# Performance work log

Hardware: AMD Instinct MI355X
Metric: run time of the kernel (lower is better)

The kernel has to match this reference:

```python
import jax, jax.numpy as jnp
from jax import lax
import numpy as np

D_MODEL = 2048
NUM_EXPERTS = 16
NUM_TOKENS = 8192  # must be divisible by NUM_EXPERTS (balanced assignment)


def setup_inputs() -> dict:
    key = jax.random.key(0)
    k1, k2 = jax.random.split(key)
    features = jax.random.normal(k1, (NUM_TOKENS, D_MODEL), dtype=jnp.float32)
    # gate weight (orthogonal init in torch; gaussian is fine for a numerical baseline)
    W = jax.random.normal(k2, (NUM_EXPERTS, D_MODEL), dtype=jnp.float32) * 0.1
    b = jnp.zeros((NUM_EXPERTS,), dtype=jnp.float32)
    return {"features": features, "W": W, "b": b, "is_training": 1}


def _balanced_assignment(scores):
    """Greedy balanced assignment: each expert receives exactly T//E tokens.
    Deterministic stand-in for the cpp auction-based balanced_assignment: scan
    over tokens, each token takes its best-scoring expert with remaining capacity.
    Returns sort_by_expert: token indices sorted (stably) by assigned expert."""
    T, E = scores.shape
    cap_per_expert = T // E

    def step(cap, s):  # cap: [E] remaining capacity, s: [E] token's scores
        masked = jnp.where(cap > 0, s, -jnp.inf)
        e = jnp.argmax(masked)
        return cap.at[e].add(-1), e

    _, tok2exp = lax.scan(step, jnp.full((E,), cap_per_expert, dtype=jnp.int32), scores)
    sort_by_expert = jnp.argsort(tok2exp, stable=True)  # [T] token ids grouped by expert
    return sort_by_expert


def reference(features, W, b, is_training):
    # gating computed under no_grad in the original
    affinities = lax.stop_gradient(features @ W.T + b)  # [T, E]
    T, E = affinities.shape
    cap = T // E

    sort_by_expert = _balanced_assignment(affinities)

    routing_probs = jax.nn.softmax(affinities, axis=1)  # [T, E]

    # gather_scores: permute probs into expert order, pick each token's score for
    # its assigned expert, then un-permute back to original token order.
    sorted_probs = routing_probs[sort_by_expert]                 # [T, E]
    expert_idx = (jnp.arange(T) // cap)[:, None]                 # [T, 1], balanced splits
    gathered = jnp.take_along_axis(sorted_probs, expert_idx, axis=1)  # [T, 1]
    i_sort = jnp.argsort(sort_by_expert)                         # inverse permutation
    gathered_scores = gathered[i_sort]                           # [T, 1]

    return sort_by_expert, gathered_scores
```

## Files before the change

### kernel.cpp

```cpp
#include <hip/hip_runtime.h>
#include <hip/hip_bf16.h>
#include <math.h>

#define T_TOK 8192
#define D_MODEL 2048
#define N_EXP 16
#define CAP 512
#define NSEG (T_TOK / 64)
#define KSPLIT 2
#define KRANGE (D_MODEL / KSPLIT)


__device__ __forceinline__ unsigned int f2ord(float f) {
    unsigned int b = __float_as_uint(f);
    return (b & 0x80000000u) ? ~b : (b | 0x80000000u);
}

__global__ __launch_bounds__(256, 2) void gemm_partial_kernel(
    const float* __restrict__ feat, const float* __restrict__ W,
    float* __restrict__ partial)
{
    __shared__ float w_lds[N_EXP * KRANGE];

    const int tid  = threadIdx.x;
    const int wave = tid >> 6, lane = tid & 63;
    const int t0   = (blockIdx.x & 255) * 32;
    const int ks   = blockIdx.x >> 8;
    const int k0   = ks * KRANGE;

    for (int i = tid; i < N_EXP * KRANGE / 4; i += 256) {
        int e = i / (KRANGE / 4), r = i % (KRANGE / 4);
        ((float4*)w_lds)[i] = *(const float4*)(W + (size_t)e * D_MODEL + k0 + r * 4);
    }
    __syncthreads();

    const float* fbase = feat + (size_t)(t0 + wave * 8) * D_MODEL + k0 + lane * 4;

    float acc[128];
    #pragma unroll
    for (int i = 0; i < 128; ++i) acc[i] = 0.f;

    float4 cur[8], nxt[8];
    #pragma unroll
    for (int r = 0; r < 8; ++r)
        cur[r] = *(const float4*)(fbase + (size_t)r * D_MODEL);

    #pragma unroll
    for (int j = 0; j < KRANGE / 256; ++j) {
        if (j < KRANGE / 256 - 1) {
            #pragma unroll
            for (int r = 0; r < 8; ++r)
                nxt[r] = *(const float4*)(fbase + (size_t)r * D_MODEL + (j + 1) * 256);
        }
        const int kbase = j * 256 + lane * 4;
        #pragma unroll
        for (int e = 0; e < N_EXP; ++e) {
            float4 wv = *(const float4*)&w_lds[e * KRANGE + kbase];
            #pragma unroll
            for (int r = 0; r < 8; ++r) {
                acc[r * 16 + e] += cur[r].x * wv.x;
                acc[r * 16 + e] += cur[r].y * wv.y;
                acc[r * 16 + e] += cur[r].z * wv.z;
                acc[r * 16 + e] += cur[r].w * wv.w;
            }
        }
        #pragma unroll
        for (int r = 0; r < 8; ++r) cur[r] = nxt[r];
    }

    #pragma unroll
    for (int step = 0; step < 6; ++step) {
        const int m    = 1 << step;
        const int half = 128 >> (step + 1);
        const bool hi  = (lane & m) != 0;
        #pragma unroll
        for (int jj = 0; jj < half; ++jj) {
            float send = hi ? acc[jj] : acc[jj + half];
            float recv = __shfl_xor(send, m, 64);
            acc[jj] = (hi ? acc[jj + half] : acc[jj]) + recv;
        }
    }
    const int rl = ((lane & 1) << 5) | (((lane >> 1) & 1) << 4) | (((lane >> 2) & 1) << 3)
                 | (((lane >> 3) & 1) << 2) | (((lane >> 4) & 1) << 1) | ((lane >> 5) & 1);
    #pragma unroll
    for (int jj = 0; jj < 2; ++jj) {
        int slot = (rl << 1) | jj;
        int r = slot >> 4, e = slot & 15;
        partial[((size_t)ks * T_TOK + t0 + wave * 8 + r) * N_EXP + e] = acc[jj];
    }
}

__global__ __launch_bounds__(256) void finalize_kernel(
    const float* __restrict__ partial, const float* __restrict__ bias,
    unsigned long long* __restrict__ pref, float* __restrict__ probs,
    unsigned char* __restrict__ choice0, int* __restrict__ cnt0)
{
    const int tid = threadIdx.x;
    const int t = blockIdx.x * 256 + tid;
    const int wave = tid >> 6, lane = tid & 63;

    float aff[N_EXP];
    {
        const float4* p0 = (const float4*)(partial + (size_t)t * N_EXP);
        const float4* p1 = (const float4*)(partial + ((size_t)T_TOK + t) * N_EXP);
        #pragma unroll
        for (int q = 0; q < 4; ++q) {
            float4 a = p0[q], b = p1[q];
            aff[q*4+0] = a.x + b.x; aff[q*4+1] = a.y + b.y;
            aff[q*4+2] = a.z + b.z; aff[q*4+3] = a.w + b.w;
        }
    }
    #pragma unroll
    for (int e = 0; e < N_EXP; ++e) aff[e] += bias[e];

    float m = aff[0];
    #pragma unroll
    for (int e = 1; e < N_EXP; ++e) m = fmaxf(m, aff[e]);
    float s = 0.f;
    #pragma unroll
    for (int e = 0; e < N_EXP; ++e) s += __expf(aff[e] - m);

    float4* pr = (float4*)(probs + (size_t)t * N_EXP);
    #pragma unroll
    for (int q = 0; q < 4; ++q) {
        float4 v;
        v.x = __expf(aff[q*4+0] - m) / s;
        v.y = __expf(aff[q*4+1] - m) / s;
        v.z = __expf(aff[q*4+2] - m) / s;
        v.w = __expf(aff[q*4+3] - m) / s;
        pr[q] = v;
    }

    unsigned long long key[N_EXP];
    #pragma unroll
    for (int j = 0; j < N_EXP; ++j)
        key[j] = ((unsigned long long)f2ord(aff[j]) << 4) | (unsigned long long)(15 - j);
    unsigned long long pk = 0ull;
    unsigned int used = 0;
    for (int r = 0; r < N_EXP; ++r) {
        unsigned long long bk = 0ull; int be = 0;
        for (int j = 0; j < N_EXP; ++j)
            if (!((used >> j) & 1u) && key[j] > bk) { bk = key[j]; be = j; }
        used |= (1u << be);
        pk = (pk << 4) | (unsigned long long)be;
    }
    pref[t] = pk;

    const int c = (int)(pk >> 60);
    choice0[t] = (unsigned char)c;
    #pragma unroll
    for (int e = 0; e < N_EXP; ++e) {
        unsigned long long mm = __ballot(c == e);
        if (lane == e) cnt0[(blockIdx.x * 4 + wave) * N_EXP + e] = (int)__popcll(mm);
    }
}

__global__ __launch_bounds__(512) void events_kernel(
    const unsigned long long* __restrict__ pref,
    const unsigned char* __restrict__ choice0,
    const int* __restrict__ cnt0, int* __restrict__ evt)
{
    __shared__ unsigned char choiceL[T_TOK];
    __shared__ int cnt [NSEG][N_EXP + 1];
    __shared__ int pseg[NSEG][N_EXP + 1];
    __shared__ int rem_cap[N_EXP], fparr[N_EXP], addF[N_EXP];
    __shared__ int s_avail, s_start, s_pmin, s_fe, s_seglo;
    __shared__ int evp[N_EXP], evf[N_EXP];

    const int tid  = threadIdx.x;
    const int wave = tid >> 6, lane = tid & 63;
    const unsigned long long lt_mask = (1ull << lane) - 1ull;

    for (int i = tid; i < T_TOK / 4; i += 512)
        ((unsigned int*)choiceL)[i] = ((const unsigned int*)choice0)[i];
    for (int i = tid; i < NSEG * N_EXP; i += 512)
        cnt[i >> 4][i & 15] = cnt0[i];
    if (tid < N_EXP) rem_cap[tid] = CAP;
    if (tid == 0) { s_avail = 0xFFFF; s_start = 0; s_seglo = 0; }
    __syncthreads();

    for (int round = 0; round < N_EXP; ++round) {
        const int start = s_start;
        const unsigned int avail = (unsigned int)s_avail;
        const int seglo = s_seglo;

        #pragma unroll
        for (int ee = 0; ee < 2; ++ee) {
            const int e = wave + ee * 8;
            const int s0 = 2 * lane, s1 = s0 + 1;
            const int c0 = (s0 >= seglo) ? cnt[s0][e] : 0;
            const int c1 = (s1 >= seglo) ? cnt[s1][e] : 0;
            const int pairsum = c0 + c1;
            int v = pairsum;
            #pragma unroll
            for (int d = 1; d < 64; d <<= 1) {
                int o = __shfl_up(v, d, 64);
                if (lane >= d) v += o;
            }
            const int excl0 = v - pairsum;
            const int excl1 = excl0 + c0;
            pseg[s0][e] = excl0;
            pseg[s1][e] = excl1;

            int fp = 0x7FFFFFFF;
            if ((avail >> e) & 1u) {
                const int need = rem_cap[e];
                int segc = 0x7FFFFFFF, kk = 0;
                if (excl0 < need && excl0 + c0 >= need)      { segc = s0; kk = need - excl0; }
                else if (excl1 < need && excl1 + c1 >= need) { segc = s1; kk = need - excl1; }
                unsigned long long b = __ballot(segc != 0x7FFFFFFF);
                if (b) {
                    int l2    = __builtin_ctzll(b);
                    int sstar = __shfl(segc, l2, 64);
                    int k2    = __shfl(kk,   l2, 64);
                    int t = sstar * 64 + lane;
                    int cc = (t >= start) ? (int)choiceL[t] : -1;
                    unsigned long long m = __ballot(cc == e);
                    int r = (int)__popcll(m & lt_mask);
                    bool hit = ((m >> lane) & 1ull) && (r == k2 - 1);
                    unsigned long long hb = __ballot(hit);
                    fp = sstar * 64 + __builtin_ctzll(hb);
                }
            }
            if (lane == 0) fparr[e] = fp;
        }
        __syncthreads();

        if (tid == 0) {
            int pm = 0x7FFFFFFF, f = 0;
            #pragma unroll
            for (int e = 0; e < N_EXP; ++e)
                if (fparr[e] < pm) { pm = fparr[e]; f = e; }
            s_pmin = pm; s_fe = f;
        }
        __syncthreads();
        const int pmin = s_pmin, fe = s_fe;
        const int segF = pmin >> 6;

        if (wave == 0) {
            int t = segF * 64 + lane;
            int cc = (t >= start && t <= pmin) ? (int)choiceL[t] : -1;
            #pragma unroll
            for (int e = 0; e < N_EXP; ++e) {
                unsigned long long mm = __ballot(cc == e);
                if (lane == e) addF[e] = (int)__popcll(mm);
            }
        }
        __syncthreads();

        if (tid < N_EXP) rem_cap[tid] -= pseg[segF][tid] + addF[tid];
        if (tid == 0) {
            evp[round] = pmin; evf[round] = fe;
            s_avail = (int)(avail & ~(1u << fe));
            s_start = pmin + 1;
            s_seglo = segF;
        }
        __syncthreads();

        if (round < N_EXP - 1) {
            const unsigned int navail = (unsigned int)s_avail;
            for (int t = pmin + 1 + tid; t < T_TOK; t += 512) {
                if ((int)choiceL[t] == fe) {
                    unsigned long long pp = pref[t];
                    int e2 = (int)(pp >> 60);
                    while (!((navail >> e2) & 1u)) { pp <<= 4; e2 = (int)(pp >> 60); }
                    choiceL[t] = (unsigned char)e2;
                }
            }
            __syncthreads();
            for (int s = segF + wave; s < NSEG; s += 8) {
                int t = s * 64 + lane;
                int cc = (t > pmin) ? (int)choiceL[t] : -1;
                #pragma unroll
                for (int e = 0; e < N_EXP; ++e) {
                    unsigned long long mm = __ballot(cc == e);
                    if (lane == e) cnt[s][e] = (int)__popcll(mm);
                }
            }
            __syncthreads();
        }
    }

    if (tid < N_EXP) { evt[tid] = evp[tid]; evt[N_EXP + tid] = evf[tid]; }
}

__global__ __launch_bounds__(256) void choice_kernel(
    const unsigned long long* __restrict__ pref, const int* __restrict__ evt,
    unsigned char* __restrict__ t2e, int* __restrict__ bcnt)
{
    __shared__ int evp[N_EXP], evf[N_EXP];
    __shared__ int sc[4][N_EXP];
    const int tid = threadIdx.x, b = blockIdx.x;
    const int wave = tid >> 6, lane = tid & 63;
    if (tid < N_EXP) evp[tid] = evt[tid];
    else if (tid < 2 * N_EXP) evf[tid - N_EXP] = evt[tid];
    __syncthreads();

    const int t = b * 256 + tid;
    unsigned int mask = 0xFFFFu;
    #pragma unroll
    for (int j = 0; j < N_EXP; ++j)
        if (evp[j] < t) mask &= ~(1u << evf[j]);

    unsigned long long pp = pref[t];
    int e = (int)(pp >> 60);
    while (!((mask >> e) & 1u)) { pp <<= 4; e = (int)(pp >> 60); }
    t2e[t] = (unsigned char)e;

    #pragma unroll
    for (int e2 = 0; e2 < N_EXP; ++e2) {
        unsigned long long mm = __ballot(e == e2);
        if (lane == e2) sc[wave][e2] = (int)__popcll(mm);
    }
    __syncthreads();
    if (tid < N_EXP)
        bcnt[b * N_EXP + tid] = sc[0][tid] + sc[1][tid] + sc[2][tid] + sc[3][tid];
}

__global__ __launch_bounds__(256) void writeout_kernel(
    const unsigned char* __restrict__ t2e, const int* __restrict__ bcnt,
    const float* __restrict__ probs,
    float* __restrict__ out0, float* __restrict__ out1)
{
    __shared__ int base[N_EXP];
    __shared__ int sc[4][N_EXP];
    const int tid = threadIdx.x, b = blockIdx.x;
    const int wave = tid >> 6, lane = tid & 63;
    const unsigned long long lt_mask = (1ull << lane) - 1ull;

    const int t = b * 256 + tid;
    const int c = (int)t2e[t];

    unsigned long long own = 0ull;
    #pragma unroll
    for (int e2 = 0; e2 < N_EXP; ++e2) {
        unsigned long long mm = __ballot(c == e2);
        if (c == e2) own = mm;
        if (lane == e2) sc[wave][e2] = (int)__popcll(mm);
    }
    if (tid < N_EXP) {
        int s = 0;
        for (int b2 = 0; b2 < b; ++b2) s += bcnt[b2 * N_EXP + tid];
        base[tid] = s;
    }
    __syncthreads();

    int rank = (int)__popcll(own & lt_mask);
    for (int w2 = 0; w2 < wave; ++w2) rank += sc[w2][c];
    const int pos = base[c] + rank;
    out0[c * CAP + pos] = (float)t;
    out1[t] = probs[(size_t)t * N_EXP + c];
}

extern "C" void kernel_launch(void* const* d_in, const int* in_sizes, int n_in,
                              void* d_out, int out_size, void* d_ws, size_t ws_size,
                              hipStream_t stream) {
    const float* feat = (const float*)d_in[0];
    const float* W    = (const float*)d_in[1];
    const float* bias = (const float*)d_in[2];

    float* out = (float*)d_out;
    char*  ws  = (char*)d_ws;

    float* partial           = (float*)ws;
    unsigned long long* pref = (unsigned long long*)(ws + 1048576);
    float* probs             = (float*)(ws + 1114112);
    unsigned char* choice0   = (unsigned char*)(ws + 1638400);
    int* cnt0                = (int*)(ws + 1646592);
    int* evt                 = (int*)(ws + 1654784);
    unsigned char* t2e       = (unsigned char*)(ws + 1654912);
    int* bcnt                = (int*)(ws + 1663104);

    hipLaunchKernelGGL(gemm_partial_kernel, dim3(512), dim3(256), 0, stream,
                       feat, W, partial);
    hipLaunchKernelGGL(finalize_kernel, dim3(T_TOK / 256), dim3(256), 0, stream,
                       partial, bias, pref, probs, choice0, cnt0);
    hipLaunchKernelGGL(events_kernel, dim3(1), dim3(512), 0, stream,
                       pref, choice0, cnt0, evt);
    hipLaunchKernelGGL(choice_kernel, dim3(T_TOK / 256), dim3(256), 0, stream,
                       pref, evt, t2e, bcnt);
    hipLaunchKernelGGL(writeout_kernel, dim3(T_TOK / 256), dim3(256), 0, stream,
                       t2e, bcnt, probs, out, out + T_TOK);
}
```

Baseline: 197.8 us.

## Track per-segment expert bitmasks in events kernel and drop GEMM K-split

The single-block events kernel now keeps per-expert 64-bit token bitmasks per segment in LDS, updated with atomicOr when tokens are reassigned. This replaces the byte choice array and the full recount of every segment with ballots each round, cutting the serial per-round work in the one-block critical path. The GEMM no longer splits K in two or stages W in LDS. Each wave does four tokens over the full K range and reads W straight from global/cache, with higher occupancy and no partial-sum buffer, so finalize reads one affinity array. The risk is LDS atomic contention and heavier W traffic through cache.

Result: faster. 191.6 us (-3.1%).

```diff
diff --git a/kernel.cpp b/kernel.cpp
--- a/kernel.cpp
+++ b/kernel.cpp
@@ -7,8 +7,6 @@
 #define N_EXP 16
 #define CAP 512
 #define NSEG (T_TOK / 64)
-#define KSPLIT 2
-#define KRANGE (D_MODEL / KSPLIT)
 
 
 __device__ __forceinline__ unsigned int f2ord(float f) {
@@ -16,62 +14,57 @@
     return (b & 0x80000000u) ? ~b : (b | 0x80000000u);
 }
 
-__global__ __launch_bounds__(256, 2) void gemm_partial_kernel(
+__global__ __launch_bounds__(256, 4) void gemm_aff_kernel(
     const float* __restrict__ feat, const float* __restrict__ W,
-    float* __restrict__ partial)
-{
-    __shared__ float w_lds[N_EXP * KRANGE];
-
+    float* __restrict__ aff)
+{
     const int tid  = threadIdx.x;
     const int wave = tid >> 6, lane = tid & 63;
-    const int t0   = (blockIdx.x & 255) * 32;
-    const int ks   = blockIdx.x >> 8;
-    const int k0   = ks * KRANGE;
-
-    for (int i = tid; i < N_EXP * KRANGE / 4; i += 256) {
-        int e = i / (KRANGE / 4), r = i % (KRANGE / 4);
-        ((float4*)w_lds)[i] = *(const float4*)(W + (size_t)e * D_MODEL + k0 + r * 4);
-    }
-    __syncthreads();
-
-    const float* fbase = feat + (size_t)(t0 + wave * 8) * D_MODEL + k0 + lane * 4;
-
-    float acc[128];
-    #pragma unroll
-    for (int i = 0; i < 128; ++i) acc[i] = 0.f;
-
-    float4 cur[8], nxt[8];
-    #pragma unroll
-    for (int r = 0; r < 8; ++r)
+    const int tbase = blockIdx.x * 16 + wave * 4;
+
+    const float* fbase = feat + (size_t)tbase * D_MODEL + lane * 4;
+
+    float acc[64];
+    #pragma unroll
+    for (int i = 0; i < 64; ++i) acc[i] = 0.f;
+
+    float4 cur[4], nxt[4];
+    #pragma unroll
+    for (int r = 0; r < 4; ++r)
         cur[r] = *(const float4*)(fbase + (size_t)r * D_MODEL);
 
     #pragma unroll
-    for (int j = 0; j < KRANGE / 256; ++j) {
-        if (j < KRANGE / 256 - 1) {
-            #pragma unroll
-            for (int r = 0; r < 8; ++r)
+    for (int j = 0; j < 8; ++j) {
+        if (j < 7) {
+            #pragma unroll
+            for (int r = 0; r < 4; ++r)
                 nxt[r] = *(const float4*)(fbase + (size_t)r * D_MODEL + (j + 1) * 256);
         }
-        const int kbase = j * 256 + lane * 4;
-        #pragma unroll
-        for (int e = 0; e < N_EXP; ++e) {
-            float4 wv = *(const float4*)&w_lds[e * KRANGE + kbase];
-            #pragma unroll
-            for (int r = 0; r < 8; ++r) {
-                acc[r * 16 + e] += cur[r].x * wv.x;
-                acc[r * 16 + e] += cur[r].y * wv.y;
-                acc[r * 16 + e] += cur[r].z * wv.z;
-                acc[r * 16 + e] += cur[r].w * wv.w;
-            }
-        }
-        #pragma unroll
-        for (int r = 0; r < 8; ++r) cur[r] = nxt[r];
+        const float* wbase = W + j * 256 + lane * 4;
+        #pragma unroll
+        for (int g = 0; g < 4; ++g) {
+            float4 wv[4];
+            #pragma unroll
+            for (int i = 0; i < 4; ++i)
+                wv[i] = *(const float4*)(wbase + (size_t)(g * 4 + i) * D_MODEL);
+            #pragma unroll
+            for (int i = 0; i < 4; ++i)
+                #pragma unroll
+                for (int r = 0; r < 4; ++r) {
+                    acc[r * 16 + g * 4 + i] += cur[r].x * wv[i].x;
+                    acc[r * 16 + g * 4 + i] += cur[r].y * wv[i].y;
+                    acc[r * 16 + g * 4 + i] += cur[r].z * wv[i].z;
+                    acc[r * 16 + g * 4 + i] += cur[r].w * wv[i].w;
+                }
+        }
+        #pragma unroll
+        for (int r = 0; r < 4; ++r) cur[r] = nxt[r];
     }
 
     #pragma unroll
     for (int step = 0; step < 6; ++step) {
         const int m    = 1 << step;
-        const int half = 128 >> (step + 1);
+        const int half = 64 >> (step + 1);
         const bool hi  = (lane & m) != 0;
         #pragma unroll
         for (int jj = 0; jj < half; ++jj) {
@@ -80,35 +73,24 @@
             acc[jj] = (hi ? acc[jj + half] : acc[jj]) + recv;
         }
     }
-    const int rl = ((lane & 1) << 5) | (((lane >> 1) & 1) << 4) | (((lane >> 2) & 1) << 3)
-                 | (((lane >> 3) & 1) << 2) | (((lane >> 4) & 1) << 1) | ((lane >> 5) & 1);
-    #pragma unroll
-    for (int jj = 0; jj < 2; ++jj) {
-        int slot = (rl << 1) | jj;
-        int r = slot >> 4, e = slot & 15;
-        partial[((size_t)ks * T_TOK + t0 + wave * 8 + r) * N_EXP + e] = acc[jj];
-    }
+    const int slot = ((lane & 1) << 5) | (((lane >> 1) & 1) << 4) | (((lane >> 2) & 1) << 3)
+                   | (((lane >> 3) & 1) << 2) | (((lane >> 4) & 1) << 1) | ((lane >> 5) & 1);
+    const int r = slot >> 4, e = slot & 15;
+    aff[(size_t)(tbase + r) * N_EXP + e] = acc[0];
 }
 
 __global__ __launch_bounds__(256) void finalize_kernel(
-    const float* __restrict__ partial, const float* __restrict__ bias,
-    unsigned long long* __restrict__ pref, float* __restrict__ probs,
-    unsigned char* __restrict__ choice0, int* __restrict__ cnt0)
-{
-    const int tid = threadIdx.x;
-    const int t = blockIdx.x * 256 + tid;
-    const int wave = tid >> 6, lane = tid & 63;
+    const float* __restrict__ aff_in, const float* __restrict__ bias,
+    unsigned long long* __restrict__ pref, float* __restrict__ probs)
+{
+    const int t = blockIdx.x * 256 + threadIdx.x;
 
     float aff[N_EXP];
-    {
-        const float4* p0 = (const float4*)(partial + (size_t)t * N_EXP);
-        const float4* p1 = (const float4*)(partial + ((size_t)T_TOK + t) * N_EXP);
-        #pragma unroll
-        for (int q = 0; q < 4; ++q) {
-            float4 a = p0[q], b = p1[q];
-            aff[q*4+0] = a.x + b.x; aff[q*4+1] = a.y + b.y;
-            aff[q*4+2] = a.z + b.z; aff[q*4+3] = a.w + b.w;
-        }
+    const float4* p = (const float4*)(aff_in + (size_t)t * N_EXP);
+    #pragma unroll
+    for (int q = 0; q < 4; ++q) {
+        float4 v = p[q];
+        aff[q*4+0] = v.x; aff[q*4+1] = v.y; aff[q*4+2] = v.z; aff[q*4+3] = v.w;
     }
     #pragma unroll
     for (int e = 0; e < N_EXP; ++e) aff[e] += bias[e];
@@ -145,79 +127,78 @@
         pk = (pk << 4) | (unsigned long long)be;
     }
     pref[t] = pk;
-
-    const int c = (int)(pk >> 60);
-    choice0[t] = (unsigned char)c;
-    #pragma unroll
-    for (int e = 0; e < N_EXP; ++e) {
-        unsigned long long mm = __ballot(c == e);
-        if (lane == e) cnt0[(blockIdx.x * 4 + wave) * N_EXP + e] = (int)__popcll(mm);
-    }
 }
 
 __global__ __launch_bounds__(512) void events_kernel(
-    const unsigned long long* __restrict__ pref,
-    const unsigned char* __restrict__ choice0,
-    const int* __restrict__ cnt0, int* __restrict__ evt)
-{
-    __shared__ unsigned char choiceL[T_TOK];
-    __shared__ int cnt [NSEG][N_EXP + 1];
-    __shared__ int pseg[NSEG][N_EXP + 1];
-    __shared__ int rem_cap[N_EXP], fparr[N_EXP], addF[N_EXP];
-    __shared__ int s_avail, s_start, s_pmin, s_fe, s_seglo;
+    const unsigned long long* __restrict__ pref, int* __restrict__ evt)
+{
+    __shared__ unsigned long long prefL[T_TOK];
+    __shared__ unsigned long long segmask[N_EXP][NSEG + 1];
+    __shared__ int pseg[N_EXP][NSEG + 1];
+    __shared__ int rem_cap[N_EXP], fparr[N_EXP];
+    __shared__ int s_avail, s_pmin, s_fe, s_seglo;
     __shared__ int evp[N_EXP], evf[N_EXP];
 
     const int tid  = threadIdx.x;
     const int wave = tid >> 6, lane = tid & 63;
     const unsigned long long lt_mask = (1ull << lane) - 1ull;
 
-    for (int i = tid; i < T_TOK / 4; i += 512)
-        ((unsigned int*)choiceL)[i] = ((const unsigned int*)choice0)[i];
-    for (int i = tid; i < NSEG * N_EXP; i += 512)
-        cnt[i >> 4][i & 15] = cnt0[i];
+    for (int i = tid; i < T_TOK; i += 512) prefL[i] = pref[i];
     if (tid < N_EXP) rem_cap[tid] = CAP;
-    if (tid == 0) { s_avail = 0xFFFF; s_start = 0; s_seglo = 0; }
+    if (tid == 0) { s_avail = 0xFFFF; s_seglo = 0; }
+    __syncthreads();
+
+    for (int s = wave; s < NSEG; s += 8) {
+        int c = (int)(prefL[s * 64 + lane] >> 60);
+        #pragma unroll
+        for (int e = 0; e < N_EXP; ++e) {
+            unsigned long long mm = __ballot(c == e);
+            if (lane == e) segmask[e][s] = mm;
+        }
+    }
     __syncthreads();
 
     for (int round = 0; round < N_EXP; ++round) {
-        const int start = s_start;
         const unsigned int avail = (unsigned int)s_avail;
-        const int seglo = s_seglo;
 
         #pragma unroll
         for (int ee = 0; ee < 2; ++ee) {
             const int e = wave + ee * 8;
-            const int s0 = 2 * lane, s1 = s0 + 1;
-            const int c0 = (s0 >= seglo) ? cnt[s0][e] : 0;
-            const int c1 = (s1 >= seglo) ? cnt[s1][e] : 0;
-            const int pairsum = c0 + c1;
-            int v = pairsum;
+            const unsigned long long m0 = segmask[e][lane];
+            const unsigned long long m1 = segmask[e][64 + lane];
+            const int c0 = (int)__popcll(m0), c1 = (int)__popcll(m1);
+            int v0 = c0;
             #pragma unroll
             for (int d = 1; d < 64; d <<= 1) {
-                int o = __shfl_up(v, d, 64);
-                if (lane >= d) v += o;
+                int o = __shfl_up(v0, d, 64);
+                if (lane >= d) v0 += o;
             }
-            const int excl0 = v - pairsum;
-            const int excl1 = excl0 + c0;
-            pseg[s0][e] = excl0;
-            pseg[s1][e] = excl1;
+            const int excl0 = v0 - c0;
+            const int tot0  = __shfl(v0, 63, 64);
+            int v1 = c1;
+            #pragma unroll
+            for (int d = 1; d < 64; d <<= 1) {
+                int o = __shfl_up(v1, d, 64);
+                if (lane >= d) v1 += o;
+            }
+            const int excl1 = tot0 + v1 - c1;
+            pseg[e][lane]      = excl0;
+            pseg[e][64 + lane] = excl1;
 
             int fp = 0x7FFFFFFF;
             if ((avail >> e) & 1u) {
                 const int need = rem_cap[e];
-                int segc = 0x7FFFFFFF, kk = 0;
-                if (excl0 < need && excl0 + c0 >= need)      { segc = s0; kk = need - excl0; }
-                else if (excl1 < need && excl1 + c1 >= need) { segc = s1; kk = need - excl1; }
-                unsigned long long b = __ballot(segc != 0x7FFFFFFF);
+                int segc = -1, kk = 0;
+                if (excl0 < need && excl0 + c0 >= need)      { segc = lane;      kk = need - excl0; }
+                else if (excl1 < need && excl1 + c1 >= need) { segc = 64 + lane; kk = need - excl1; }
+                unsigned long long b = __ballot(segc >= 0);
                 if (b) {
                     int l2    = __builtin_ctzll(b);
                     int sstar = __shfl(segc, l2, 64);
                     int k2    = __shfl(kk,   l2, 64);
-                    int t = sstar * 64 + lane;
-                    int cc = (t >= start) ? (int)choiceL[t] : -1;
-                    unsigned long long m = __ballot(cc == e);
-                    int r = (int)__popcll(m & lt_mask);
-                    bool hit = ((m >> lane) & 1ull) && (r == k2 - 1);
+                    unsigned long long m = segmask[e][sstar];
+                    int rr = (int)__popcll(m & lt_mask);
+                    bool hit = ((m >> lane) & 1ull) && (rr == k2 - 1);
                     unsigned long long hb = __ballot(hit);
                     fp = sstar * 64 + __builtin_ctzll(hb);
                 }
@@ -236,49 +217,41 @@
         __syncthreads();
         const int pmin = s_pmin, fe = s_fe;
         const int segF = pmin >> 6;
-
-        if (wave == 0) {
-            int t = segF * 64 + lane;
-            int cc = (t >= start && t <= pmin) ? (int)choiceL[t] : -1;
-            #pragma unroll
-            for (int e = 0; e < N_EXP; ++e) {
-                unsigned long long mm = __ballot(cc == e);
-                if (lane == e) addF[e] = (int)__popcll(mm);
-            }
-        }
-        __syncthreads();
-
-        if (tid < N_EXP) rem_cap[tid] -= pseg[segF][tid] + addF[tid];
+        const int seglo = s_seglo;
+
+        if (tid < N_EXP) {
+            const int e = tid;
+            unsigned long long mlep = ((pmin & 63) == 63) ? ~0ull
+                                      : ((1ull << ((pmin & 63) + 1)) - 1ull);
+            unsigned long long m = segmask[e][segF];
+            rem_cap[e] -= pseg[e][segF] + (int)__popcll(m & mlep);
+            segmask[e][segF] = m & ~mlep;
+        }
+        for (int i = tid; i < (segF - seglo) * N_EXP; i += 512)
+            segmask[i & 15][seglo + (i >> 4)] = 0ull;
         if (tid == 0) {
             evp[round] = pmin; evf[round] = fe;
             s_avail = (int)(avail & ~(1u << fe));
-            s_start = pmin + 1;
             s_seglo = segF;
         }
         __syncthreads();
 
         if (round < N_EXP - 1) {
-            const unsigned int navail = (unsigned int)s_avail;
-            for (int t = pmin + 1 + tid; t < T_TOK; t += 512) {
-                if ((int)choiceL[t] == fe) {
-                    unsigned long long pp = pref[t];
-                    int e2 = (int)(pp >> 60);
-                    while (!((navail >> e2) & 1u)) { pp <<= 4; e2 = (int)(pp >> 60); }
-                    choiceL[t] = (unsigned char)e2;
+            const unsigned int navail = avail & ~(1u << fe);
+            for (int s = segF + wave; s < NSEG; s += 8) {
+                unsigned long long m = segmask[fe][s];
+                if (m) {
+                    if ((m >> lane) & 1ull) {
+                        unsigned long long pp = prefL[s * 64 + lane];
+                        int e2 = (int)(pp >> 60);
+                        while (!((navail >> e2) & 1u)) { pp <<= 4; e2 = (int)(pp >> 60); }
+                        atomicOr(&segmask[e2][s], 1ull << lane);
+                    }
+                    if (lane == 0) segmask[fe][s] = 0ull;
                 }
             }
-            __syncthreads();
-            for (int s = segF + wave; s < NSEG; s += 8) {
-                int t = s * 64 + lane;
-                int cc = (t > pmin) ? (int)choiceL[t] : -1;
-                #pragma unroll
-                for (int e = 0; e < N_EXP; ++e) {
-                    unsigned long long mm = __ballot(cc == e);
-                    if (lane == e) cnt[s][e] = (int)__popcll(mm);
-                }
-            }
-            __syncthreads();
-        }
+        }
+        __syncthreads();
     }
 
     if (tid < N_EXP) { evt[tid] = evp[tid]; evt[N_EXP + tid] = evf[tid]; }
@@ -362,21 +335,19 @@
     float* out = (float*)d_out;
     char*  ws  = (char*)d_ws;
 
-    float* partial           = (float*)ws;
-    unsigned long long* pref = (unsigned long long*)(ws + 1048576);
-    float* probs             = (float*)(ws + 1114112);
-    unsigned char* choice0   = (unsigned char*)(ws + 1638400);
-    int* cnt0                = (int*)(ws + 1646592);
-    int* evt                 = (int*)(ws + 1654784);
-    unsigned char* t2e       = (unsigned char*)(ws + 1654912);
-    int* bcnt                = (int*)(ws + 1663104);
-
-    hipLaunchKernelGGL(gemm_partial_kernel, dim3(512), dim3(256), 0, stream,
-                       feat, W, partial);
+    float* aff               = (float*)ws;
+    unsigned long long* pref = (unsigned long long*)(ws + 524288);
+    float* probs             = (float*)(ws + 589824);
+    int* evt                 = (int*)(ws + 1114112);
+    unsigned char* t2e       = (unsigned char*)(ws + 1114240);
+    int* bcnt                = (int*)(ws + 1122432);
+
+    hipLaunchKernelGGL(gemm_aff_kernel, dim3(512), dim3(256), 0, stream,
+                       feat, W, aff);
     hipLaunchKernelGGL(finalize_kernel, dim3(T_TOK / 256), dim3(256), 0, stream,
-                       partial, bias, pref, probs, choice0, cnt0);
+                       aff, bias, pref, probs);
     hipLaunchKernelGGL(events_kernel, dim3(1), dim3(512), 0, stream,
-                       pref, choice0, cnt0, evt);
+                       pref, evt);
     hipLaunchKernelGGL(choice_kernel, dim3(T_TOK / 256), dim3(256), 0, stream,
                        pref, evt, t2e, bcnt);
     hipLaunchKernelGGL(writeout_kernel, dim3(T_TOK / 256), dim3(256), 0, stream,
```
